# Kernel tuning notes

Measured on AMD Instinct MI355X. Metric: run time of the kernel, lower is better.

Reference implementation:

```python
import jax, jax.numpy as jnp
import numpy as np

N_NODES = 100000
N_EDGES = 3200000
N_GRAPHS = 1024
D_IN, D_HID, N_CLASSES = 128, 64, 10


def setup_inputs() -> dict:
    key = jax.random.key(0)
    ks = jax.random.split(key, 12)
    x = jax.random.normal(ks[0], (N_NODES, D_IN), dtype=jnp.float32)
    edge_index = jax.random.randint(ks[1], (2, N_EDGES), 0, N_NODES, dtype=jnp.int64)
    batch = jnp.sort(jax.random.randint(ks[2], (N_NODES,), 0, N_GRAPHS, dtype=jnp.int64))
    def w(k, shape, fan_in):
        return (jax.random.normal(k, shape, dtype=jnp.float32) / np.sqrt(fan_in)).astype(jnp.float32)
    return {
        "x": x,
        "edge_index": edge_index,
        "batch": batch,
        "W1": w(ks[3], (D_IN, D_HID), D_IN),  "b1": jnp.zeros((D_HID,), jnp.float32),
        "W2": w(ks[4], (D_HID, D_HID), D_HID), "b2": jnp.zeros((D_HID,), jnp.float32),
        "W3": w(ks[5], (D_HID, D_HID), D_HID), "b3": jnp.zeros((D_HID,), jnp.float32),
        "Wl": w(ks[6], (D_HID, N_CLASSES), D_HID), "bl": jnp.zeros((N_CLASSES,), jnp.float32),
    }


def _gcn_conv(x, W, b, src, dst, n_nodes):
    # GCNConv: out = D^{-1/2} (A + I) D^{-1/2} X W + b  (symmetric norm, self-loops)
    h = x @ W  # [N, D_out] - transform first (PyG order)
    loop = jnp.arange(n_nodes, dtype=src.dtype)
    s = jnp.concatenate([src, loop])  # [E+N]
    d = jnp.concatenate([dst, loop])
    deg = jax.ops.segment_sum(jnp.ones_like(d, dtype=h.dtype), d, num_segments=n_nodes)
    dinv = jnp.where(deg > 0, jax.lax.rsqrt(deg), 0.0)
    norm = dinv[s] * dinv[d]  # [E+N]
    out = jax.ops.segment_sum(h[s] * norm[:, None], d, num_segments=n_nodes)
    return out + b


def reference(x, edge_index, batch, W1, b1, W2, b2, W3, b3, Wl, bl):
    src, dst = edge_index[0], edge_index[1]
    n = x.shape[0]
    h = jax.nn.relu(_gcn_conv(x, W1, b1, src, dst, n))
    h = jax.nn.relu(_gcn_conv(h, W2, b2, src, dst, n))
    h = _gcn_conv(h, W3, b3, src, dst, n)
    # global mean pool over graphs
    sums = jax.ops.segment_sum(h, batch, num_segments=N_GRAPHS)
    cnts = jax.ops.segment_sum(jnp.ones((n,), h.dtype), batch, num_segments=N_GRAPHS)
    g = sums / jnp.maximum(cnts, 1.0)[:, None]
    # dropout is identity in eval mode
    return g @ Wl + bl  # [N_GRAPHS, N_CLASSES]
```

## Files before the change

### kernel.cpp

```cpp
#include <hip/hip_runtime.h>
#include <hip/hip_fp16.h>

#define D_IN 128
#define D_HID 64
#define N_GRAPHS 1024
#define N_CLASSES 10

#define NPB 256
#define MAXNB 1024
#define CHUNK 16384

typedef __attribute__((ext_vector_type(8))) short bf16x8;
typedef __attribute__((ext_vector_type(4))) float f32x4;

__device__ __forceinline__ unsigned bf16_rne(float f) {
    unsigned u = __float_as_uint(f);
    return (u + 0x7FFF + ((u >> 16) & 1)) >> 16;
}

__global__ __launch_bounds__(256) void hist_buckets(const int* __restrict__ dst, int nE, int NB,
                                                    int* __restrict__ bcnt) {
    __shared__ int h[MAXNB];
    for (int i = threadIdx.x; i < NB; i += 256) h[i] = 0;
    __syncthreads();
    int stride = gridDim.x * 256;
    for (int i = blockIdx.x * 256 + threadIdx.x; i < nE; i += stride)
        atomicAdd(&h[dst[i] >> 8], 1);
    __syncthreads();
    for (int i = threadIdx.x; i < NB; i += 256) {
        int c = h[i];
        if (c) atomicAdd(&bcnt[i], c);
    }
}

__global__ __launch_bounds__(1024) void scan_buckets(const int* __restrict__ bcnt, int NB, int nE,
                                                     int* __restrict__ boff, int* __restrict__ gcur) {
    __shared__ int t[1024];
    int tid = threadIdx.x;
    int v = (tid < NB) ? bcnt[tid] : 0;
    t[tid] = v;
    __syncthreads();
    for (int off = 1; off < 1024; off <<= 1) {
        int u = (tid >= off) ? t[tid - off] : 0;
        __syncthreads();
        t[tid] += u;
        __syncthreads();
    }
    int excl = t[tid] - v;
    if (tid < NB) { boff[tid] = excl; gcur[tid] = excl; }
    if (tid == 0) boff[NB] = nE;
}

__global__ __launch_bounds__(256) void bin_edges(const int* __restrict__ src, const int* __restrict__ dst,
                                                 int nE, int NB, int* __restrict__ gcur,
                                                 int* __restrict__ binned) {
    __shared__ int h[MAXNB];
    __shared__ int base[MAXNB];
    int c0 = blockIdx.x * CHUNK;
    int c1 = min(nE, c0 + CHUNK);
    for (int i = threadIdx.x; i < NB; i += 256) h[i] = 0;
    __syncthreads();
    for (int i = c0 + threadIdx.x; i < c1; i += 256) atomicAdd(&h[dst[i] >> 8], 1);
    __syncthreads();
    for (int b = threadIdx.x; b < NB; b += 256) {
        int c = h[b];
        base[b] = c ? atomicAdd(&gcur[b], c) : 0;
        h[b] = 0;
    }
    __syncthreads();
    for (int i = c0 + threadIdx.x; i < c1; i += 256) {
        int d = dst[i];
        int b = d >> 8;
        int r = atomicAdd(&h[b], 1);
        binned[base[b] + r] = src[i] | ((d & 255) << 17);
    }
}

__global__ __launch_bounds__(256) void build_csr(const int* __restrict__ boff,
                                                 const int* __restrict__ binned,
                                                 int n, int nE,
                                                 int* __restrict__ rowptr, float* __restrict__ dinv,
                                                 int* __restrict__ csr_src) {
    __shared__ int cnt[NPB];
    __shared__ int soff[NPB];
    __shared__ int cur[NPB];
    int b = blockIdx.x, tid = threadIdx.x;
    int nbase = b << 8;
    int e0 = boff[b], e1 = boff[b + 1];
    cnt[tid] = 0;
    __syncthreads();
    for (int i = e0 + tid; i < e1; i += 256) atomicAdd(&cnt[binned[i] >> 17], 1);
    __syncthreads();
    int v = cnt[tid];
    soff[tid] = v;
    __syncthreads();
    for (int off = 1; off < 256; off <<= 1) {
        int u = (tid >= off) ? soff[tid - off] : 0;
        __syncthreads();
        soff[tid] += u;
        __syncthreads();
    }
    int excl = soff[tid] - v;
    __syncthreads();
    soff[tid] = excl;
    cur[tid] = 0;
    int node = nbase + tid;
    if (node < n) {
        rowptr[node] = e0 + excl;
        dinv[node] = 1.0f / sqrtf((float)(cnt[tid] + 1));
    }
    if (b == 0 && tid == 0) rowptr[n] = nE;
    __syncthreads();
    for (int i = e0 + tid; i < e1; i += 256) {
        int e = binned[i];
        int ld = e >> 17;
        int r = atomicAdd(&cur[ld], 1);
        csr_src[e0 + soff[ld] + r] = e & 0x1FFFF;
    }
}

template <int K>
__global__ void pack_w(const float* __restrict__ W, short* __restrict__ hi, short* __restrict__ lo) {
    constexpr int SLOTS = (K / 32) * 4 * 64;
    for (int s = threadIdx.x; s < SLOTS; s += 256) {
        int lane = s & 63, nf = (s >> 6) & 3, ks = s >> 8;
        int fq = lane >> 4, fr = lane & 15;
#pragma unroll
        for (int j = 0; j < 8; ++j) {
            int k = ks * 32 + fq * 8 + j;
            int c = nf * 16 + fr;
            float v = W[k * 64 + c];
            unsigned hb = bf16_rne(v);
            float hf = __uint_as_float(hb << 16);
            float l = v - hf;
            hi[s * 8 + j] = (short)hb;
            lo[s * 8 + j] = (short)bf16_rne(l);
        }
    }
}

template <int K>
__global__ __launch_bounds__(256) void gemm_mfma(
    const float* __restrict__ X, const short* __restrict__ whi, const short* __restrict__ wlo,
    const float* __restrict__ bias, int relu, __half* __restrict__ H, int n) {
    constexpr int KS = K / 32;
    int wave = threadIdx.x >> 6, lane = threadIdx.x & 63;
    int fr = lane & 15, fq = lane >> 4;
    int rowbase = blockIdx.x * 64 + wave * 16;
    int rclamp = min(rowbase + fr, n - 1);
    f32x4 acc[4] = {{0,0,0,0},{0,0,0,0},{0,0,0,0},{0,0,0,0}};
#pragma unroll
    for (int ks = 0; ks < KS; ++ks) {
        const float* xp = X + (size_t)rclamp * K + ks * 32 + fq * 8;
        float xv[8];
        *(f32x4*)&xv[0] = *(const f32x4*)xp;
        *(f32x4*)&xv[4] = *(const f32x4*)(xp + 4);
        if (bias != nullptr) {
            const float* bp = bias + ks * 32 + fq * 8;
#pragma unroll
            for (int j = 0; j < 8; ++j) {
                float v = xv[j] + bp[j];
                if (relu) v = fmaxf(v, 0.0f);
                xv[j] = v;
            }
        }
        bf16x8 ahi, alo;
#pragma unroll
        for (int j = 0; j < 8; ++j) {
            unsigned hb = bf16_rne(xv[j]);
            float hf = __uint_as_float(hb << 16);
            ahi[j] = (short)hb;
            alo[j] = (short)bf16_rne(xv[j] - hf);
        }
        const short* whp = whi + (size_t)(ks * 4) * 64 * 8 + lane * 8;
        const short* wlp = wlo + (size_t)(ks * 4) * 64 * 8 + lane * 8;
#pragma unroll
        for (int nf = 0; nf < 4; ++nf) {
            bf16x8 bhi = *(const bf16x8*)(whp + nf * 512);
            bf16x8 blo = *(const bf16x8*)(wlp + nf * 512);
            acc[nf] = __builtin_amdgcn_mfma_f32_16x16x32_bf16(ahi, bhi, acc[nf], 0, 0, 0);
            acc[nf] = __builtin_amdgcn_mfma_f32_16x16x32_bf16(alo, bhi, acc[nf], 0, 0, 0);
            acc[nf] = __builtin_amdgcn_mfma_f32_16x16x32_bf16(ahi, blo, acc[nf], 0, 0, 0);
        }
    }
#pragma unroll
    for (int nf = 0; nf < 4; ++nf) {
#pragma unroll
        for (int reg = 0; reg < 4; ++reg) {
            int r = rowbase + fq * 4 + reg;
            if (r < n) H[((size_t)r << 6) + nf * 16 + fr] = __float2half(acc[nf][reg]);
        }
    }
}

__global__ __launch_bounds__(256) void gather_agg(
    const int* __restrict__ rowptr, const int* __restrict__ csr_src,
    const float* __restrict__ dinv, const __half* __restrict__ A,
    float* __restrict__ B, int n) {
    int gtid = blockIdx.x * 256 + threadIdx.x;
    int wid = gtid >> 6, lane = gtid & 63;
    int nw = (gridDim.x * 256) >> 6;
    int slot = lane >> 4, fl = lane & 15;
    for (int d = wid; d < n; d += nw) {
        float dd = dinv[d];
        int e0 = rowptr[d], e1 = rowptr[d + 1];
        float4 acc = make_float4(0.f, 0.f, 0.f, 0.f);
        if (slot == 0) {
            uint2 q = *(const uint2*)(A + ((size_t)d << 6) + (fl << 2));
            float2 f0 = __half22float2(*(__half2*)&q.x);
            float2 f1 = __half22float2(*(__half2*)&q.y);
            float w = dd * dd;
            acc = make_float4(w * f0.x, w * f0.y, w * f1.x, w * f1.y);
        }
        int e = e0 + slot;
        for (; e + 4 < e1; e += 8) {
            int s0 = csr_src[e], s1 = csr_src[e + 4];
            float w0 = dd * dinv[s0], w1 = dd * dinv[s1];
            uint2 q0 = *(const uint2*)(A + ((size_t)s0 << 6) + (fl << 2));
            uint2 q1 = *(const uint2*)(A + ((size_t)s1 << 6) + (fl << 2));
            float2 a0 = __half22float2(*(__half2*)&q0.x);
            float2 a1 = __half22float2(*(__half2*)&q0.y);
            float2 b0 = __half22float2(*(__half2*)&q1.x);
            float2 b1 = __half22float2(*(__half2*)&q1.y);
            acc.x = fmaf(w0, a0.x, acc.x); acc.y = fmaf(w0, a0.y, acc.y);
            acc.z = fmaf(w0, a1.x, acc.z); acc.w = fmaf(w0, a1.y, acc.w);
            acc.x = fmaf(w1, b0.x, acc.x); acc.y = fmaf(w1, b0.y, acc.y);
            acc.z = fmaf(w1, b1.x, acc.z); acc.w = fmaf(w1, b1.y, acc.w);
        }
        if (e < e1) {
            int s = csr_src[e];
            float w = dd * dinv[s];
            uint2 q = *(const uint2*)(A + ((size_t)s << 6) + (fl << 2));
            float2 a0 = __half22float2(*(__half2*)&q.x);
            float2 a1 = __half22float2(*(__half2*)&q.y);
            acc.x = fmaf(w, a0.x, acc.x); acc.y = fmaf(w, a0.y, acc.y);
            acc.z = fmaf(w, a1.x, acc.z); acc.w = fmaf(w, a1.y, acc.w);
        }
        acc.x += __shfl_xor(acc.x, 16); acc.y += __shfl_xor(acc.y, 16);
        acc.z += __shfl_xor(acc.z, 16); acc.w += __shfl_xor(acc.w, 16);
        acc.x += __shfl_xor(acc.x, 32); acc.y += __shfl_xor(acc.y, 32);
        acc.z += __shfl_xor(acc.z, 32); acc.w += __shfl_xor(acc.w, 32);
        if (slot == 0) *(float4*)(B + ((size_t)d << 6) + (fl << 2)) = acc;
    }
}

__global__ __launch_bounds__(256) void pool_nodes(
    const float* __restrict__ B, const float* __restrict__ b3,
    const int* __restrict__ batch, float* __restrict__ sums,
    float* __restrict__ gcnt, int n, int chunk) {
    int gtid = blockIdx.x * blockDim.x + threadIdx.x;
    int wid = gtid >> 6, lane = gtid & 63;
    int start = wid * chunk;
    if (start >= n) return;
    int end = min(n, start + chunk);
    float bl3 = b3[lane];
    int curg = batch[start];
    float acc = 0.0f;
    int cl = 0;
    for (int node = start; node < end; ++node) {
        int g = batch[node];
        if (g != curg) {
            atomicAdd(&sums[((size_t)curg << 6) + lane], acc);
            if (lane == 0) atomicAdd(&gcnt[curg], (float)cl);
            acc = 0.0f; cl = 0; curg = g;
        }
        acc += B[((size_t)node << 6) + lane] + bl3;
        ++cl;
    }
    atomicAdd(&sums[((size_t)curg << 6) + lane], acc);
    if (lane == 0) atomicAdd(&gcnt[curg], (float)cl);
}

__global__ void final_linear(const float* __restrict__ sums, const float* __restrict__ gcnt,
                             const float* __restrict__ Wl, const float* __restrict__ bl,
                             float* __restrict__ out) {
    int idx = blockIdx.x * blockDim.x + threadIdx.x;
    if (idx >= N_GRAPHS * N_CLASSES) return;
    int g = idx / N_CLASSES, c = idx - g * N_CLASSES;
    float inv = 1.0f / fmaxf(gcnt[g], 1.0f);
    float acc = bl[c];
#pragma unroll
    for (int d = 0; d < D_HID; ++d)
        acc = fmaf(sums[(g << 6) + d] * inv, Wl[d * N_CLASSES + c], acc);
    out[idx] = acc;
}

extern "C" void kernel_launch(void* const* d_in, const int* in_sizes, int n_in,
                              void* d_out, int out_size, void* d_ws, size_t ws_size,
                              hipStream_t stream) {
    const float* x     = (const float*)d_in[0];
    const int*   ei    = (const int*)d_in[1];
    const int*   batch = (const int*)d_in[2];
    const float* W1 = (const float*)d_in[3];
    const float* b1 = (const float*)d_in[4];
    const float* W2 = (const float*)d_in[5];
    const float* b2 = (const float*)d_in[6];
    const float* W3 = (const float*)d_in[7];
    const float* b3 = (const float*)d_in[8];
    const float* Wl = (const float*)d_in[9];
    const float* bl = (const float*)d_in[10];

    int n = in_sizes[0] / D_IN;
    int E = in_sizes[1] / 2;
    const int* src = ei;
    const int* dst = ei + E;
    int NB = (n + NPB - 1) / NPB;

    size_t off = 0;
    auto alloc = [&](size_t bytes) {
        void* p = (char*)d_ws + off;
        off += ((bytes + 255) & ~(size_t)255);
        return p;
    };
    int*    rowptr  = (int*)alloc(((size_t)n + 1) * 4);
    int*    bcnt    = (int*)alloc(MAXNB * 4);
    int*    boff    = (int*)alloc((MAXNB + 1) * 4);
    int*    gcur    = (int*)alloc(MAXNB * 4);
    int*    binned  = (int*)alloc((size_t)E * 4);
    int*    csr_src = (int*)alloc((size_t)E * 4);
    float*  dinv    = (float*)alloc((size_t)n * 4);
    float*  B       = (float*)alloc((size_t)n * 64 * 4);
    float*  sums    = (float*)alloc(N_GRAPHS * 64 * 4);
    float*  gcnt    = (float*)alloc(N_GRAPHS * 4);
    short*  w1hi    = (short*)alloc(4 * 4 * 64 * 8 * 2);
    short*  w1lo    = (short*)alloc(4 * 4 * 64 * 8 * 2);
    short*  w2hi    = (short*)alloc(2 * 4 * 64 * 8 * 2);
    short*  w2lo    = (short*)alloc(2 * 4 * 64 * 8 * 2);
    short*  w3hi    = (short*)alloc(2 * 4 * 64 * 8 * 2);
    short*  w3lo    = (short*)alloc(2 * 4 * 64 * 8 * 2);
    __half* A       = (__half*)binned;

    int blk = 256;
    int gBin  = (E + CHUNK - 1) / CHUNK;
    int gGemm = (n + 63) / 64;

    hipMemsetAsync(bcnt, 0, MAXNB * sizeof(int), stream);
    hist_buckets<<<256, blk, 0, stream>>>(dst, E, NB, bcnt);
    scan_buckets<<<1, 1024, 0, stream>>>(bcnt, NB, E, boff, gcur);
    bin_edges<<<gBin, blk, 0, stream>>>(src, dst, E, NB, gcur, binned);
    build_csr<<<NB, blk, 0, stream>>>(boff, binned, n, E, rowptr, dinv, csr_src);

    pack_w<D_IN><<<1, blk, 0, stream>>>(W1, w1hi, w1lo);
    pack_w<D_HID><<<1, blk, 0, stream>>>(W2, w2hi, w2lo);
    pack_w<D_HID><<<1, blk, 0, stream>>>(W3, w3hi, w3lo);

    gemm_mfma<D_IN><<<gGemm, blk, 0, stream>>>(x, w1hi, w1lo, nullptr, 0, A, n);
    gather_agg<<<2048, blk, 0, stream>>>(rowptr, csr_src, dinv, A, B, n);

    gemm_mfma<D_HID><<<gGemm, blk, 0, stream>>>(B, w2hi, w2lo, b1, 1, A, n);
    gather_agg<<<2048, blk, 0, stream>>>(rowptr, csr_src, dinv, A, B, n);

    gemm_mfma<D_HID><<<gGemm, blk, 0, stream>>>(B, w3hi, w3lo, b2, 1, A, n);
    gather_agg<<<2048, blk, 0, stream>>>(rowptr, csr_src, dinv, A, B, n);

    hipMemsetAsync(sums, 0, (N_GRAPHS * 64 + N_GRAPHS) * sizeof(float), stream);
    {
        int waves = 256 * 256 / 64;
        int chunk = (n + waves - 1) / waves;
        pool_nodes<<<256, blk, 0, stream>>>(B, b3, batch, sums, gcnt, n, chunk);
    }
    final_linear<<<(N_GRAPHS * N_CLASSES + blk - 1) / blk, blk, 0, stream>>>(
        sums, gcnt, Wl, bl, (float*)d_out);
}
```

Measured before the change: 399.4 us.

## Split feature matrices into 16-column quarters and gather each quarter separately

Stores the GEMM outputs and aggregation buffers as four column-quarter planes of 16 features each. Aggregation becomes four passes, each gathering 32-byte half-precision rows, so each pass's gathered table is a quarter of the size and more likely to stay in cache. This targets the cache misses of random neighbour gathers, at the cost of re-reading the CSR indices and dinv four times and launching more kernels. It also shrinks the edge-binning chunk and enlarges the histogram grid.

```diff
diff --git a/kernel.cpp b/kernel.cpp
--- a/kernel.cpp
+++ b/kernel.cpp
@@ -8,7 +8,7 @@
 
 #define NPB 256
 #define MAXNB 1024
-#define CHUNK 16384
+#define CHUNK 4096
 
 typedef __attribute__((ext_vector_type(8))) short bf16x8;
 typedef __attribute__((ext_vector_type(4))) float f32x4;
@@ -139,7 +139,7 @@
     }
 }
 
-template <int K>
+template <int K, int SPLIT_IN>
 __global__ __launch_bounds__(256) void gemm_mfma(
     const float* __restrict__ X, const short* __restrict__ whi, const short* __restrict__ wlo,
     const float* __restrict__ bias, int relu, __half* __restrict__ H, int n) {
@@ -151,12 +151,17 @@
     f32x4 acc[4] = {{0,0,0,0},{0,0,0,0},{0,0,0,0},{0,0,0,0}};
 #pragma unroll
     for (int ks = 0; ks < KS; ++ks) {
-        const float* xp = X + (size_t)rclamp * K + ks * 32 + fq * 8;
+        int kbase = ks * 32 + fq * 8;
+        const float* xp;
+        if (SPLIT_IN)
+            xp = X + (size_t)(kbase >> 4) * n * 16 + (size_t)rclamp * 16 + (kbase & 15);
+        else
+            xp = X + (size_t)rclamp * K + kbase;
         float xv[8];
         *(f32x4*)&xv[0] = *(const f32x4*)xp;
         *(f32x4*)&xv[4] = *(const f32x4*)(xp + 4);
         if (bias != nullptr) {
-            const float* bp = bias + ks * 32 + fq * 8;
+            const float* bp = bias + kbase;
 #pragma unroll
             for (int j = 0; j < 8; ++j) {
                 float v = xv[j] + bp[j];
@@ -188,36 +193,36 @@
 #pragma unroll
         for (int reg = 0; reg < 4; ++reg) {
             int r = rowbase + fq * 4 + reg;
-            if (r < n) H[((size_t)r << 6) + nf * 16 + fr] = __float2half(acc[nf][reg]);
-        }
-    }
-}
-
-__global__ __launch_bounds__(256) void gather_agg(
+            if (r < n) H[(size_t)nf * n * 16 + (size_t)r * 16 + fr] = __float2half(acc[nf][reg]);
+        }
+    }
+}
+
+__global__ __launch_bounds__(256) void gather_q(
     const int* __restrict__ rowptr, const int* __restrict__ csr_src,
-    const float* __restrict__ dinv, const __half* __restrict__ A,
-    float* __restrict__ B, int n) {
+    const float* __restrict__ dinv, const __half* __restrict__ Aq,
+    float* __restrict__ Bq, int n) {
     int gtid = blockIdx.x * 256 + threadIdx.x;
     int wid = gtid >> 6, lane = gtid & 63;
     int nw = (gridDim.x * 256) >> 6;
-    int slot = lane >> 4, fl = lane & 15;
+    int slot = lane >> 2, fl = lane & 3;
     for (int d = wid; d < n; d += nw) {
         float dd = dinv[d];
         int e0 = rowptr[d], e1 = rowptr[d + 1];
         float4 acc = make_float4(0.f, 0.f, 0.f, 0.f);
         if (slot == 0) {
-            uint2 q = *(const uint2*)(A + ((size_t)d << 6) + (fl << 2));
+            uint2 q = *(const uint2*)(Aq + (size_t)d * 16 + (fl << 2));
             float2 f0 = __half22float2(*(__half2*)&q.x);
             float2 f1 = __half22float2(*(__half2*)&q.y);
             float w = dd * dd;
             acc = make_float4(w * f0.x, w * f0.y, w * f1.x, w * f1.y);
         }
         int e = e0 + slot;
-        for (; e + 4 < e1; e += 8) {
-            int s0 = csr_src[e], s1 = csr_src[e + 4];
+        for (; e + 16 < e1; e += 32) {
+            int s0 = csr_src[e], s1 = csr_src[e + 16];
             float w0 = dd * dinv[s0], w1 = dd * dinv[s1];
-            uint2 q0 = *(const uint2*)(A + ((size_t)s0 << 6) + (fl << 2));
-            uint2 q1 = *(const uint2*)(A + ((size_t)s1 << 6) + (fl << 2));
+            uint2 q0 = *(const uint2*)(Aq + (size_t)s0 * 16 + (fl << 2));
+            uint2 q1 = *(const uint2*)(Aq + (size_t)s1 * 16 + (fl << 2));
             float2 a0 = __half22float2(*(__half2*)&q0.x);
             float2 a1 = __half22float2(*(__half2*)&q0.y);
             float2 b0 = __half22float2(*(__half2*)&q1.x);
@@ -230,17 +235,18 @@
         if (e < e1) {
             int s = csr_src[e];
             float w = dd * dinv[s];
-            uint2 q = *(const uint2*)(A + ((size_t)s << 6) + (fl << 2));
+            uint2 q = *(const uint2*)(Aq + (size_t)s * 16 + (fl << 2));
             float2 a0 = __half22float2(*(__half2*)&q.x);
             float2 a1 = __half22float2(*(__half2*)&q.y);
             acc.x = fmaf(w, a0.x, acc.x); acc.y = fmaf(w, a0.y, acc.y);
             acc.z = fmaf(w, a1.x, acc.z); acc.w = fmaf(w, a1.y, acc.w);
         }
-        acc.x += __shfl_xor(acc.x, 16); acc.y += __shfl_xor(acc.y, 16);
-        acc.z += __shfl_xor(acc.z, 16); acc.w += __shfl_xor(acc.w, 16);
-        acc.x += __shfl_xor(acc.x, 32); acc.y += __shfl_xor(acc.y, 32);
-        acc.z += __shfl_xor(acc.z, 32); acc.w += __shfl_xor(acc.w, 32);
-        if (slot == 0) *(float4*)(B + ((size_t)d << 6) + (fl << 2)) = acc;
+#pragma unroll
+        for (int m = 4; m <= 32; m <<= 1) {
+            acc.x += __shfl_xor(acc.x, m); acc.y += __shfl_xor(acc.y, m);
+            acc.z += __shfl_xor(acc.z, m); acc.w += __shfl_xor(acc.w, m);
+        }
+        if (slot == 0) *(float4*)(Bq + (size_t)d * 16 + (fl << 2)) = acc;
     }
 }
 
@@ -253,6 +259,7 @@
     int start = wid * chunk;
     if (start >= n) return;
     int end = min(n, start + chunk);
+    const float* Bl = B + (size_t)(lane >> 4) * n * 16 + (lane & 15);
     float bl3 = b3[lane];
     int curg = batch[start];
     float acc = 0.0f;
@@ -264,7 +271,7 @@
             if (lane == 0) atomicAdd(&gcnt[curg], (float)cl);
             acc = 0.0f; cl = 0; curg = g;
         }
-        acc += B[((size_t)node << 6) + lane] + bl3;
+        acc += Bl[(size_t)node * 16] + bl3;
         ++cl;
     }
     atomicAdd(&sums[((size_t)curg << 6) + lane], acc);
@@ -333,9 +340,11 @@
     int blk = 256;
     int gBin  = (E + CHUNK - 1) / CHUNK;
     int gGemm = (n + 63) / 64;
+    size_t qA = (size_t)n * 16;
+    size_t qB = (size_t)n * 16;
 
     hipMemsetAsync(bcnt, 0, MAXNB * sizeof(int), stream);
-    hist_buckets<<<256, blk, 0, stream>>>(dst, E, NB, bcnt);
+    hist_buckets<<<1024, blk, 0, stream>>>(dst, E, NB, bcnt);
     scan_buckets<<<1, 1024, 0, stream>>>(bcnt, NB, E, boff, gcur);
     bin_edges<<<gBin, blk, 0, stream>>>(src, dst, E, NB, gcur, binned);
     build_csr<<<NB, blk, 0, stream>>>(boff, binned, n, E, rowptr, dinv, csr_src);
@@ -344,14 +353,17 @@
     pack_w<D_HID><<<1, blk, 0, stream>>>(W2, w2hi, w2lo);
     pack_w<D_HID><<<1, blk, 0, stream>>>(W3, w3hi, w3lo);
 
-    gemm_mfma<D_IN><<<gGemm, blk, 0, stream>>>(x, w1hi, w1lo, nullptr, 0, A, n);
-    gather_agg<<<2048, blk, 0, stream>>>(rowptr, csr_src, dinv, A, B, n);
-
-    gemm_mfma<D_HID><<<gGemm, blk, 0, stream>>>(B, w2hi, w2lo, b1, 1, A, n);
-    gather_agg<<<2048, blk, 0, stream>>>(rowptr, csr_src, dinv, A, B, n);
-
-    gemm_mfma<D_HID><<<gGemm, blk, 0, stream>>>(B, w3hi, w3lo, b2, 1, A, n);
-    gather_agg<<<2048, blk, 0, stream>>>(rowptr, csr_src, dinv, A, B, n);
+    gemm_mfma<D_IN, 0><<<gGemm, blk, 0, stream>>>(x, w1hi, w1lo, nullptr, 0, A, n);
+    for (int q = 0; q < 4; ++q)
+        gather_q<<<2048, blk, 0, stream>>>(rowptr, csr_src, dinv, A + q * qA, B + q * qB, n);
+
+    gemm_mfma<D_HID, 1><<<gGemm, blk, 0, stream>>>(B, w2hi, w2lo, b1, 1, A, n);
+    for (int q = 0; q < 4; ++q)
+        gather_q<<<2048, blk, 0, stream>>>(rowptr, csr_src, dinv, A + q * qA, B + q * qB, n);
+
+    gemm_mfma<D_HID, 1><<<gGemm, blk, 0, stream>>>(B, w3hi, w3lo, b2, 1, A, n);
+    for (int q = 0; q < 4; ++q)
+        gather_q<<<2048, blk, 0, stream>>>(rowptr, csr_src, dinv, A + q * qA, B + q * qB, n);
 
     hipMemsetAsync(sums, 0, (N_GRAPHS * 64 + N_GRAPHS) * sizeof(float), stream);
     {
```

Result: slower. 682.9 us (+71.0%).
